# Kernel tuning notes

Hardware: AMD Instinct MI355X
Metric: run time of the kernel (lower is better)

Reference implementation:

```python
import jax, jax.numpy as jnp
import numpy as np

N_NODES = 50000
N_EDGES = 600000
D_IN = 44


def _glorot(key, shape):
    fan_in = shape[0]
    return jax.random.normal(key, shape, jnp.float32) * (1.0 / np.sqrt(fan_in))


def setup_inputs() -> dict:
    key = jax.random.key(0)
    ks = jax.random.split(key, 12)
    x = jax.random.normal(ks[0], (N_NODES, D_IN), jnp.float32)
    edge_index = jax.random.randint(ks[1], (2, N_EDGES), 0, N_NODES, dtype=jnp.int64)
    return {
        "x": x,
        "edge_index": edge_index,
        "W1": _glorot(ks[2], (D_IN, 128)),  "b1": jnp.zeros((128,), jnp.float32),
        "W2": _glorot(ks[3], (128, 64)),    "b2": jnp.zeros((64,), jnp.float32),
        "W3": _glorot(ks[4], (64, 32)),     "b3": jnp.zeros((32,), jnp.float32),
        "Wf1": _glorot(ks[5], (32, 16)),    "bf1": jnp.zeros((16,), jnp.float32),
        "Wf2": _glorot(ks[6], (16, 1)),     "bf2": jnp.zeros((1,), jnp.float32),
    }


def _gcn_conv(x, W, b, src, dst, norm, n):
    # GCNConv: h = x @ W; out_i = sum_{j->i} norm_ij * h_j  (self-loops included in src/dst)
    h = x @ W
    msg = h[src] * norm[:, None]              # [E+N, d_out] gather + scale
    out = jax.ops.segment_sum(msg, dst, num_segments=n)  # scatter-add
    return out + b


def reference(x, edge_index, W1, b1, W2, b2, W3, b3, Wf1, bf1, Wf2, bf2):
    n = x.shape[0]
    loop = jnp.arange(n, dtype=edge_index.dtype)
    src = jnp.concatenate([edge_index[0], loop])
    dst = jnp.concatenate([edge_index[1], loop])
    # symmetric normalization deg^-1/2 A_hat deg^-1/2 (deg includes self-loops)
    deg = jax.ops.segment_sum(jnp.ones_like(dst, dtype=x.dtype), dst, num_segments=n)
    dinv = jax.lax.rsqrt(jnp.maximum(deg, 1.0))
    norm = dinv[src] * dinv[dst]

    h = jax.nn.relu(_gcn_conv(x, W1, b1, src, dst, norm, n))
    h = jax.nn.relu(_gcn_conv(h, W2, b2, src, dst, norm, n))
    h = jax.nn.relu(_gcn_conv(h, W3, b3, src, dst, norm, n))
    h = jax.nn.relu(h @ Wf1 + bf1)
    return jax.nn.sigmoid(h @ Wf2 + bf2)
```

## Files before the change

kernel.cpp:

```cpp
#include <hip/hip_runtime.h>
#include <hip/hip_bf16.h>
#include <hip/hip_fp16.h>
#include <math.h>

#define N_NODES 50000
#define N_EDGES 600000
#define D_IN    44


__device__ __forceinline__ unsigned pack_bf2(float a, float b) {
    unsigned ua = __float_as_uint(a);
    ua = (ua + 0x7fffu + ((ua >> 16) & 1u)) >> 16;
    unsigned ub = __float_as_uint(b);
    ub = (ub + 0x7fffu + ((ub >> 16) & 1u)) & 0xffff0000u;
    return ua | ub;
}


__global__ void k_zero(int* p, int n) {
    int i = blockIdx.x * blockDim.x + threadIdx.x;
    if (i < n) p[i] = 0;
}

__global__ void k_count(const int* __restrict__ dst, int* degc, int e) {
    int i = blockIdx.x * blockDim.x + threadIdx.x;
    if (i < e) atomicAdd(&degc[dst[i]], 1);
}

__global__ void k_blocksum(const int* __restrict__ degc, int* __restrict__ bsum, int n) {
    int i = blockIdx.x * 256 + threadIdx.x;
    int v = (i < n) ? degc[i] : 0;
    #pragma unroll
    for (int off = 32; off > 0; off >>= 1) v += __shfl_down(v, off, 64);
    __shared__ int ws[4];
    if ((threadIdx.x & 63) == 0) ws[threadIdx.x >> 6] = v;
    __syncthreads();
    if (threadIdx.x == 0) bsum[blockIdx.x] = ws[0] + ws[1] + ws[2] + ws[3];
}

__global__ void k_scanbsum(int* bsum, int nb) {
    __shared__ int s[256];
    int t = threadIdx.x;
    int v = (t < nb) ? bsum[t] : 0;
    s[t] = v;
    __syncthreads();
    #pragma unroll
    for (int off = 1; off < 256; off <<= 1) {
        int u = (t >= off) ? s[t - off] : 0;
        __syncthreads();
        s[t] += u;
        __syncthreads();
    }
    if (t < nb) bsum[t] = (t == 0) ? 0 : s[t - 1];
}

__global__ void k_rowptr(const int* __restrict__ degc, const int* __restrict__ bsum,
                         int* __restrict__ row_ptr, int* __restrict__ cursor,
                         float* __restrict__ dinv, int n) {
    __shared__ int s[256];
    int i = blockIdx.x * 256 + threadIdx.x;
    int t = threadIdx.x;
    int d = (i < n) ? degc[i] : 0;
    s[t] = d;
    __syncthreads();
    #pragma unroll
    for (int off = 1; off < 256; off <<= 1) {
        int u = (t >= off) ? s[t - off] : 0;
        __syncthreads();
        s[t] += u;
        __syncthreads();
    }
    int ex = s[t] - d + bsum[blockIdx.x];
    if (i < n) {
        row_ptr[i] = ex;
        cursor[i]  = ex;
        dinv[i]    = rsqrtf(1.0f + (float)d);
        if (i == n - 1) row_ptr[n] = ex + d;
    }
}

__global__ void k_fill(const int* __restrict__ src, const int* __restrict__ dst,
                       const float* __restrict__ dinv, int* cursor,
                       unsigned* __restrict__ csr_ew, int e) {
    int i = blockIdx.x * blockDim.x + threadIdx.x;
    if (i < e) {
        int s = src[i], d = dst[i];
        int p = atomicAdd(&cursor[d], 1);
        __half h = __float2half(dinv[s] * dinv[d]);
        csr_ew[p] = (unsigned)s | ((unsigned)__half_as_ushort(h) << 16);
    }
}

__global__ void k_packx(const float* __restrict__ x, unsigned* __restrict__ xh, int npairs) {
    int i = blockIdx.x * blockDim.x + threadIdx.x;
    if (i < npairs) {
        float2 v = ((const float2*)x)[i];
        xh[i] = pack_bf2(v.x, v.y);
    }
}


#define AGG_BODY(T2, W4, g, j, acc)                                             \
    {                                                                           \
        int lo = row_ptr[g], hi = row_ptr[(g) + 1];                             \
        for (int k = lo; k < hi; k += 8) {                                      \
            unsigned e0 = csr_ew[min(k + 0, hi - 1)];                           \
            unsigned e1 = csr_ew[min(k + 1, hi - 1)];                           \
            unsigned e2 = csr_ew[min(k + 2, hi - 1)];                           \
            unsigned e3 = csr_ew[min(k + 3, hi - 1)];                           \
            unsigned e4 = csr_ew[min(k + 4, hi - 1)];                           \
            unsigned e5 = csr_ew[min(k + 5, hi - 1)];                           \
            unsigned e6 = csr_ew[min(k + 6, hi - 1)];                           \
            unsigned e7 = csr_ew[min(k + 7, hi - 1)];                           \
            float w0 = __half2float(__ushort_as_half((unsigned short)(e0 >> 16)));                     \
            float w1 = (k + 1 < hi) ? __half2float(__ushort_as_half((unsigned short)(e1 >> 16))) : 0.0f;\
            float w2 = (k + 2 < hi) ? __half2float(__ushort_as_half((unsigned short)(e2 >> 16))) : 0.0f;\
            float w3 = (k + 3 < hi) ? __half2float(__ushort_as_half((unsigned short)(e3 >> 16))) : 0.0f;\
            float w4 = (k + 4 < hi) ? __half2float(__ushort_as_half((unsigned short)(e4 >> 16))) : 0.0f;\
            float w5 = (k + 5 < hi) ? __half2float(__ushort_as_half((unsigned short)(e5 >> 16))) : 0.0f;\
            float w6 = (k + 6 < hi) ? __half2float(__ushort_as_half((unsigned short)(e6 >> 16))) : 0.0f;\
            float w7 = (k + 7 < hi) ? __half2float(__ushort_as_half((unsigned short)(e7 >> 16))) : 0.0f;\
            uint2 t0 = T2[(size_t)(e0 & 0xffffu) * (W4) + (j)];                 \
            uint2 t1 = T2[(size_t)(e1 & 0xffffu) * (W4) + (j)];                 \
            uint2 t2 = T2[(size_t)(e2 & 0xffffu) * (W4) + (j)];                 \
            uint2 t3 = T2[(size_t)(e3 & 0xffffu) * (W4) + (j)];                 \
            uint2 t4 = T2[(size_t)(e4 & 0xffffu) * (W4) + (j)];                 \
            uint2 t5 = T2[(size_t)(e5 & 0xffffu) * (W4) + (j)];                 \
            uint2 t6 = T2[(size_t)(e6 & 0xffffu) * (W4) + (j)];                 \
            uint2 t7 = T2[(size_t)(e7 & 0xffffu) * (W4) + (j)];                 \
            AGG_ACC(t0, w0) AGG_ACC(t1, w1) AGG_ACC(t2, w2) AGG_ACC(t3, w3)     \
            AGG_ACC(t4, w4) AGG_ACC(t5, w5) AGG_ACC(t6, w6) AGG_ACC(t7, w7)     \
        }                                                                       \
    }

#define AGG_ACC(tv, wv)                                   \
        acc.x += wv * __uint_as_float(tv.x << 16);        \
        acc.y += wv * __uint_as_float(tv.x & 0xffff0000u);\
        acc.z += wv * __uint_as_float(tv.y << 16);        \
        acc.w += wv * __uint_as_float(tv.y & 0xffff0000u);


__global__ void k_agg1(const unsigned* __restrict__ T, const float* __restrict__ dinv,
                       const int* __restrict__ row_ptr, const unsigned* __restrict__ csr_ew,
                       unsigned short* __restrict__ O, int n) {
    int idx = blockIdx.x * 256 + threadIdx.x;
    if (idx >= n * 11) return;
    int g = idx / 11;
    int j = idx - g * 11;

    const uint2* T2 = (const uint2*)T;
    float di = dinv[g];
    float sw = di * di;
    uint2 sv = T2[(size_t)g * 11 + j];
    float4 acc;
    acc.x = sw * __uint_as_float(sv.x << 16);
    acc.y = sw * __uint_as_float(sv.x & 0xffff0000u);
    acc.z = sw * __uint_as_float(sv.y << 16);
    acc.w = sw * __uint_as_float(sv.y & 0xffff0000u);
    AGG_BODY(T2, 11, g, j, acc)
    uint2 o;
    o.x = pack_bf2(acc.x, acc.y);
    o.y = pack_bf2(acc.z, acc.w);
    ((uint2*)O)[(size_t)g * 11 + j] = o;
}


template<int DI, int DO, int CT, bool BIAS_RELU, bool IN_BF16, bool OUT_BF16>
__global__ void k_gemm(const void* __restrict__ Xv, const float* __restrict__ W,
                       const float* __restrict__ b, void* __restrict__ H, int n) {
    const int ct0 = blockIdx.y * CT;
    int node = blockIdx.x * blockDim.x + threadIdx.x;
    if (node >= n) return;

    float acc[CT];
    #pragma unroll
    for (int c = 0; c < CT; ++c) acc[c] = BIAS_RELU ? b[ct0 + c] : 0.0f;

    const float* Wb = W + ct0;
    #pragma unroll
    for (int k0 = 0; k0 < DI / 4; ++k0) {
        float x0, x1, x2, x3;
        if (IN_BF16) {
            uint2 xv = ((const uint2*)((const unsigned short*)Xv + (size_t)node * DI))[k0];
            x0 = __uint_as_float(xv.x << 16);
            x1 = __uint_as_float(xv.x & 0xffff0000u);
            x2 = __uint_as_float(xv.y << 16);
            x3 = __uint_as_float(xv.y & 0xffff0000u);
        } else {
            float4 xv = ((const float4*)((const float*)Xv + (size_t)node * DI))[k0];
            x0 = xv.x; x1 = xv.y; x2 = xv.z; x3 = xv.w;
        }
        #pragma unroll
        for (int c = 0; c < CT; ++c) acc[c] += x0 * Wb[(k0 * 4 + 0) * DO + c];
        #pragma unroll
        for (int c = 0; c < CT; ++c) acc[c] += x1 * Wb[(k0 * 4 + 1) * DO + c];
        #pragma unroll
        for (int c = 0; c < CT; ++c) acc[c] += x2 * Wb[(k0 * 4 + 2) * DO + c];
        #pragma unroll
        for (int c = 0; c < CT; ++c) acc[c] += x3 * Wb[(k0 * 4 + 3) * DO + c];
    }

    #pragma unroll
    for (int c4 = 0; c4 < CT / 4; ++c4) {
        float4 v;
        v.x = acc[c4 * 4 + 0]; v.y = acc[c4 * 4 + 1];
        v.z = acc[c4 * 4 + 2]; v.w = acc[c4 * 4 + 3];
        if (BIAS_RELU) {
            v.x = fmaxf(v.x, 0.0f); v.y = fmaxf(v.y, 0.0f);
            v.z = fmaxf(v.z, 0.0f); v.w = fmaxf(v.w, 0.0f);
        }
        if (OUT_BF16) {
            uint2 p;
            p.x = pack_bf2(v.x, v.y);
            p.y = pack_bf2(v.z, v.w);
            ((uint2*)((unsigned short*)H + (size_t)node * DO + ct0))[c4] = p;
        } else {
            ((float4*)((float*)H + (size_t)node * DO + ct0))[c4] = v;
        }
    }
}


__global__ void __launch_bounds__(64) k_fused23(
        const unsigned* __restrict__ T, const float* __restrict__ dinv,
        const int* __restrict__ row_ptr, const unsigned* __restrict__ csr_ew,
        const float* __restrict__ b2, const float* __restrict__ W3,
        unsigned short* __restrict__ outH, int n) {
    __shared__ float Xs[4 * 68];
    const int m = threadIdx.x / 16;
    const int j = threadIdx.x % 16;
    const int g = blockIdx.x * 4 + m;
    const int gm = min(g, n - 1);

    const uint2* T2 = (const uint2*)T;
    {
        float di = dinv[gm];
        float sw = di * di;
        uint2 sv = T2[(size_t)gm * 16 + j];
        float4 acc;
        acc.x = sw * __uint_as_float(sv.x << 16);
        acc.y = sw * __uint_as_float(sv.x & 0xffff0000u);
        acc.z = sw * __uint_as_float(sv.y << 16);
        acc.w = sw * __uint_as_float(sv.y & 0xffff0000u);
        AGG_BODY(T2, 16, gm, j, acc)
        float4 bv = ((const float4*)b2)[j];
        acc.x = fmaxf(acc.x + bv.x, 0.0f);
        acc.y = fmaxf(acc.y + bv.y, 0.0f);
        acc.z = fmaxf(acc.z + bv.z, 0.0f);
        acc.w = fmaxf(acc.w + bv.w, 0.0f);
        *(float4*)&Xs[m * 68 + 4 * j] = acc;
    }
    __syncthreads();

    {
        const int c = j * 2;
        float ax = 0.0f, ay = 0.0f;
        #pragma unroll 4
        for (int k4 = 0; k4 < 16; ++k4) {
            float4 hv = *(const float4*)&Xs[m * 68 + 4 * k4];
#define F3_STEP(hs, kk) { \
            float2 wv = *(const float2*)&W3[(kk) * 32 + c]; \
            ax += (hs) * wv.x; ay += (hs) * wv.y; }
            F3_STEP(hv.x, 4 * k4 + 0)
            F3_STEP(hv.y, 4 * k4 + 1)
            F3_STEP(hv.z, 4 * k4 + 2)
            F3_STEP(hv.w, 4 * k4 + 3)
#undef F3_STEP
        }
        if (g < n) *(unsigned*)(outH + (size_t)g * 32 + c) = pack_bf2(ax, ay);
    }
}


__global__ void __launch_bounds__(64) k_fused3m(
        const unsigned* __restrict__ T, const float* __restrict__ dinv,
        const int* __restrict__ row_ptr, const unsigned* __restrict__ csr_ew,
        const float* __restrict__ b3,
        const float* __restrict__ Wf1, const float* __restrict__ bf1,
        const float* __restrict__ Wf2, const float* __restrict__ bf2,
        float* __restrict__ out, int n) {
    __shared__ float Xs[8 * 36];
    const int m = threadIdx.x / 8;
    const int j = threadIdx.x % 8;
    const int g = blockIdx.x * 8 + m;
    const int gm = min(g, n - 1);

    const uint2* T2 = (const uint2*)T;
    {
        float di = dinv[gm];
        float sw = di * di;
        uint2 sv = T2[(size_t)gm * 8 + j];
        float4 acc;
        acc.x = sw * __uint_as_float(sv.x << 16);
        acc.y = sw * __uint_as_float(sv.x & 0xffff0000u);
        acc.z = sw * __uint_as_float(sv.y << 16);
        acc.w = sw * __uint_as_float(sv.y & 0xffff0000u);
        AGG_BODY(T2, 8, gm, j, acc)
        float4 bv = ((const float4*)b3)[j];
        acc.x = fmaxf(acc.x + bv.x, 0.0f);
        acc.y = fmaxf(acc.y + bv.y, 0.0f);
        acc.z = fmaxf(acc.z + bv.z, 0.0f);
        acc.w = fmaxf(acc.w + bv.w, 0.0f);
        *(float4*)&Xs[m * 36 + 4 * j] = acc;
    }
    __syncthreads();

    {
        const int c = j * 2;
        float h0 = bf1[c], h1 = bf1[c + 1];
        #pragma unroll
        for (int k = 0; k < 32; ++k) {
            float xs = Xs[m * 36 + k];
            float2 wv = *(const float2*)&Wf1[k * 16 + c];
            h0 += xs * wv.x;
            h1 += xs * wv.y;
        }
        float2 w2 = *(const float2*)&Wf2[c];
        float partial = fmaxf(h0, 0.0f) * w2.x + fmaxf(h1, 0.0f) * w2.y;
        partial += __shfl_down(partial, 4);
        partial += __shfl_down(partial, 2);
        partial += __shfl_down(partial, 1);
        if (j == 0 && g < n) out[g] = 1.0f / (1.0f + expf(-(partial + bf2[0])));
    }
}


extern "C" void kernel_launch(void* const* d_in, const int* in_sizes, int n_in,
                              void* d_out, int out_size, void* d_ws, size_t ws_size,
                              hipStream_t stream) {
    const float* x   = (const float*)d_in[0];
    const int*   ei  = (const int*)d_in[1];
    const float* W1  = (const float*)d_in[2];
    const float* b1  = (const float*)d_in[3];
    const float* W2  = (const float*)d_in[4];
    const float* b2  = (const float*)d_in[5];
    const float* W3  = (const float*)d_in[6];
    const float* b3  = (const float*)d_in[7];
    const float* Wf1 = (const float*)d_in[8];
    const float* bf1 = (const float*)d_in[9];
    const float* Wf2 = (const float*)d_in[10];
    const float* bf2 = (const float*)d_in[11];
    float* out = (float*)d_out;

    const int N = N_NODES, E = N_EDGES;
    const int* src = ei;
    const int* dst = ei + E;

    const int B   = 256;
    const int NB  = (N + B - 1) / B;
    const int NBX = 200;

    char* w = (char*)d_ws;
    float*    dinv    = (float*)w;     w += (size_t)N * 4;
    int*      degc    = (int*)w;       w += (size_t)N * 4;
    int*      row_ptr = (int*)w;       w += (size_t)(N + 4) * 4;
    int*      cursor  = (int*)w;       w += (size_t)N * 4;
    int*      bsum    = (int*)w;       w += (size_t)256 * 4;
    unsigned* csr_ew  = (unsigned*)w;  w += (size_t)E * 4;
    unsigned* xh      = (unsigned*)w;  w += (size_t)N * 44 * 2;
    unsigned short* aggXh = (unsigned short*)w;  w += (size_t)N * 44 * 2;
    float*    buf1    = (float*)w;     w += (size_t)N * 128 * 4;
    unsigned short* bufAh = (unsigned short*)w;  w += (size_t)N * 64 * 2;
    unsigned short* bufBh = (unsigned short*)w;  w += (size_t)N * 32 * 2;

    k_zero     <<<NB, B, 0, stream>>>(degc, N);
    k_packx    <<<(N * 22 + B - 1) / B, B, 0, stream>>>(x, xh, N * 22);
    k_count    <<<(E + B - 1) / B, B, 0, stream>>>(dst, degc, E);
    k_blocksum <<<NB, B, 0, stream>>>(degc, bsum, N);
    k_scanbsum <<<1, B, 0, stream>>>(bsum, NB);
    k_rowptr   <<<NB, B, 0, stream>>>(degc, bsum, row_ptr, cursor, dinv, N);
    k_fill     <<<(E + B - 1) / B, B, 0, stream>>>(src, dst, dinv, cursor, csr_ew, E);

    k_agg1<<<(N * 11 + B - 1) / B, B, 0, stream>>>(xh, dinv, row_ptr, csr_ew, aggXh, N);
    k_gemm<44, 128, 16, true, true, false><<<dim3(NBX, 8), B, 0, stream>>>(aggXh, W1, b1, buf1, N);
    k_gemm<128, 64, 16, false, false, true><<<dim3(NBX, 4), B, 0, stream>>>(buf1, W2, nullptr, bufAh, N);

    k_fused23<<<(N + 3) / 4, 64, 0, stream>>>((const unsigned*)bufAh, dinv, row_ptr,
                                              csr_ew, b2, W3, bufBh, N);

    k_fused3m<<<(N + 7) / 8, 64, 0, stream>>>((const unsigned*)bufBh, dinv, row_ptr,
                                              csr_ew, b3, Wf1, bf1, Wf2, bf2, out, N);
}
```

Measured before the change: 263.1 us.

## Widen aggregation gathers to 16-byte loads, enlarge fused blocks, merge setup kernels

In the layer-2/3 fused kernels, each thread now gathers a uint4 (8 bf16 values) per neighbour instead of a uint2, which halves the threads per node. Blocks are enlarged to 32 nodes each, and each thread computes 4 output columns in the small GEMM epilogue. Separately, the degree zeroing is folded into the x-packing kernel and the block-sum scan into the row-pointer kernel, removing two launches. The tradeoffs are more registers per thread and a redundant 256-wide scan in every row-pointer block.

```diff
diff --git a/kernel.cpp b/kernel.cpp
--- a/kernel.cpp
+++ b/kernel.cpp
@@ -16,10 +16,18 @@
     return ua | ub;
 }
 
-
-__global__ void k_zero(int* p, int n) {
+#define BL(u) __uint_as_float((u) << 16)
+#define BH(u) __uint_as_float((u) & 0xffff0000u)
+
+
+__global__ void k_packx(const float* __restrict__ x, unsigned* __restrict__ xh,
+                        int npairs, int* __restrict__ degc, int n) {
     int i = blockIdx.x * blockDim.x + threadIdx.x;
-    if (i < n) p[i] = 0;
+    if (i < npairs) {
+        float2 v = ((const float2*)x)[i];
+        xh[i] = pack_bf2(v.x, v.y);
+    }
+    if (i < n) degc[i] = 0;
 }
 
 __global__ void k_count(const int* __restrict__ dst, int* degc, int e) {
@@ -38,11 +46,28 @@
     if (threadIdx.x == 0) bsum[blockIdx.x] = ws[0] + ws[1] + ws[2] + ws[3];
 }
 
-__global__ void k_scanbsum(int* bsum, int nb) {
+__global__ void k_rowptr(const int* __restrict__ degc, const int* __restrict__ bsum,
+                         int* __restrict__ row_ptr, int* __restrict__ cursor,
+                         float* __restrict__ dinv, int n, int nb) {
+    __shared__ int sb[256];
     __shared__ int s[256];
     int t = threadIdx.x;
-    int v = (t < nb) ? bsum[t] : 0;
-    s[t] = v;
+
+    int bv = (t < nb) ? bsum[t] : 0;
+    sb[t] = bv;
+    __syncthreads();
+    #pragma unroll
+    for (int off = 1; off < 256; off <<= 1) {
+        int u = (t >= off) ? sb[t - off] : 0;
+        __syncthreads();
+        sb[t] += u;
+        __syncthreads();
+    }
+    int prefix = (blockIdx.x == 0) ? 0 : sb[blockIdx.x - 1];
+
+    int i = blockIdx.x * 256 + t;
+    int d = (i < n) ? degc[i] : 0;
+    s[t] = d;
     __syncthreads();
     #pragma unroll
     for (int off = 1; off < 256; off <<= 1) {
@@ -51,26 +76,7 @@
         s[t] += u;
         __syncthreads();
     }
-    if (t < nb) bsum[t] = (t == 0) ? 0 : s[t - 1];
-}
-
-__global__ void k_rowptr(const int* __restrict__ degc, const int* __restrict__ bsum,
-                         int* __restrict__ row_ptr, int* __restrict__ cursor,
-                         float* __restrict__ dinv, int n) {
-    __shared__ int s[256];
-    int i = blockIdx.x * 256 + threadIdx.x;
-    int t = threadIdx.x;
-    int d = (i < n) ? degc[i] : 0;
-    s[t] = d;
-    __syncthreads();
-    #pragma unroll
-    for (int off = 1; off < 256; off <<= 1) {
-        int u = (t >= off) ? s[t - off] : 0;
-        __syncthreads();
-        s[t] += u;
-        __syncthreads();
-    }
-    int ex = s[t] - d + bsum[blockIdx.x];
+    int ex = s[t] - d + prefix;
     if (i < n) {
         row_ptr[i] = ex;
         cursor[i]  = ex;
@@ -88,14 +94,6 @@
         int p = atomicAdd(&cursor[d], 1);
         __half h = __float2half(dinv[s] * dinv[d]);
         csr_ew[p] = (unsigned)s | ((unsigned)__half_as_ushort(h) << 16);
-    }
-}
-
-__global__ void k_packx(const float* __restrict__ x, unsigned* __restrict__ xh, int npairs) {
-    int i = blockIdx.x * blockDim.x + threadIdx.x;
-    if (i < npairs) {
-        float2 v = ((const float2*)x)[i];
-        xh[i] = pack_bf2(v.x, v.y);
     }
 }
 
@@ -134,10 +132,50 @@
     }
 
 #define AGG_ACC(tv, wv)                                   \
-        acc.x += wv * __uint_as_float(tv.x << 16);        \
-        acc.y += wv * __uint_as_float(tv.x & 0xffff0000u);\
-        acc.z += wv * __uint_as_float(tv.y << 16);        \
-        acc.w += wv * __uint_as_float(tv.y & 0xffff0000u);
+        acc.x += wv * BL(tv.x);                           \
+        acc.y += wv * BH(tv.x);                           \
+        acc.z += wv * BL(tv.y);                           \
+        acc.w += wv * BH(tv.y);
+
+
+#define AGG_ACC4(tv, wv)                                  \
+        a0.x += wv * BL(tv.x); a0.y += wv * BH(tv.x);     \
+        a0.z += wv * BL(tv.y); a0.w += wv * BH(tv.y);     \
+        a1.x += wv * BL(tv.z); a1.y += wv * BH(tv.z);     \
+        a1.z += wv * BL(tv.w); a1.w += wv * BH(tv.w);
+
+#define AGG_BODY4(T4, W4, g, j)                                                 \
+    {                                                                           \
+        int lo = row_ptr[g], hi = row_ptr[(g) + 1];                             \
+        for (int k = lo; k < hi; k += 8) {                                      \
+            unsigned e0 = csr_ew[min(k + 0, hi - 1)];                           \
+            unsigned e1 = csr_ew[min(k + 1, hi - 1)];                           \
+            unsigned e2 = csr_ew[min(k + 2, hi - 1)];                           \
+            unsigned e3 = csr_ew[min(k + 3, hi - 1)];                           \
+            unsigned e4 = csr_ew[min(k + 4, hi - 1)];                           \
+            unsigned e5 = csr_ew[min(k + 5, hi - 1)];                           \
+            unsigned e6 = csr_ew[min(k + 6, hi - 1)];                           \
+            unsigned e7 = csr_ew[min(k + 7, hi - 1)];                           \
+            float w0 = __half2float(__ushort_as_half((unsigned short)(e0 >> 16)));                     \
+            float w1 = (k + 1 < hi) ? __half2float(__ushort_as_half((unsigned short)(e1 >> 16))) : 0.0f;\
+            float w2 = (k + 2 < hi) ? __half2float(__ushort_as_half((unsigned short)(e2 >> 16))) : 0.0f;\
+            float w3 = (k + 3 < hi) ? __half2float(__ushort_as_half((unsigned short)(e3 >> 16))) : 0.0f;\
+            float w4 = (k + 4 < hi) ? __half2float(__ushort_as_half((unsigned short)(e4 >> 16))) : 0.0f;\
+            float w5 = (k + 5 < hi) ? __half2float(__ushort_as_half((unsigned short)(e5 >> 16))) : 0.0f;\
+            float w6 = (k + 6 < hi) ? __half2float(__ushort_as_half((unsigned short)(e6 >> 16))) : 0.0f;\
+            float w7 = (k + 7 < hi) ? __half2float(__ushort_as_half((unsigned short)(e7 >> 16))) : 0.0f;\
+            uint4 t0 = T4[(size_t)(e0 & 0xffffu) * (W4) + (j)];                 \
+            uint4 t1 = T4[(size_t)(e1 & 0xffffu) * (W4) + (j)];                 \
+            uint4 t2 = T4[(size_t)(e2 & 0xffffu) * (W4) + (j)];                 \
+            uint4 t3 = T4[(size_t)(e3 & 0xffffu) * (W4) + (j)];                 \
+            uint4 t4 = T4[(size_t)(e4 & 0xffffu) * (W4) + (j)];                 \
+            uint4 t5 = T4[(size_t)(e5 & 0xffffu) * (W4) + (j)];                 \
+            uint4 t6 = T4[(size_t)(e6 & 0xffffu) * (W4) + (j)];                 \
+            uint4 t7 = T4[(size_t)(e7 & 0xffffu) * (W4) + (j)];                 \
+            AGG_ACC4(t0, w0) AGG_ACC4(t1, w1) AGG_ACC4(t2, w2) AGG_ACC4(t3, w3) \
+            AGG_ACC4(t4, w4) AGG_ACC4(t5, w5) AGG_ACC4(t6, w6) AGG_ACC4(t7, w7) \
+        }                                                                       \
+    }
 
 
 __global__ void k_agg1(const unsigned* __restrict__ T, const float* __restrict__ dinv,
@@ -153,10 +191,10 @@
     float sw = di * di;
     uint2 sv = T2[(size_t)g * 11 + j];
     float4 acc;
-    acc.x = sw * __uint_as_float(sv.x << 16);
-    acc.y = sw * __uint_as_float(sv.x & 0xffff0000u);
-    acc.z = sw * __uint_as_float(sv.y << 16);
-    acc.w = sw * __uint_as_float(sv.y & 0xffff0000u);
+    acc.x = sw * BL(sv.x);
+    acc.y = sw * BH(sv.x);
+    acc.z = sw * BL(sv.y);
+    acc.w = sw * BH(sv.y);
     AGG_BODY(T2, 11, g, j, acc)
     uint2 o;
     o.x = pack_bf2(acc.x, acc.y);
@@ -182,10 +220,7 @@
         float x0, x1, x2, x3;
         if (IN_BF16) {
             uint2 xv = ((const uint2*)((const unsigned short*)Xv + (size_t)node * DI))[k0];
-            x0 = __uint_as_float(xv.x << 16);
-            x1 = __uint_as_float(xv.x & 0xffff0000u);
-            x2 = __uint_as_float(xv.y << 16);
-            x3 = __uint_as_float(xv.y & 0xffff0000u);
+            x0 = BL(xv.x); x1 = BH(xv.x); x2 = BL(xv.y); x3 = BH(xv.y);
         } else {
             float4 xv = ((const float4*)((const float*)Xv + (size_t)node * DI))[k0];
             x0 = xv.x; x1 = xv.y; x2 = xv.z; x3 = xv.w;
@@ -221,106 +256,118 @@
 }
 
 
-__global__ void __launch_bounds__(64) k_fused23(
+__global__ void __launch_bounds__(256) k_fused23(
         const unsigned* __restrict__ T, const float* __restrict__ dinv,
         const int* __restrict__ row_ptr, const unsigned* __restrict__ csr_ew,
         const float* __restrict__ b2, const float* __restrict__ W3,
         unsigned short* __restrict__ outH, int n) {
-    __shared__ float Xs[4 * 68];
-    const int m = threadIdx.x / 16;
-    const int j = threadIdx.x % 16;
-    const int g = blockIdx.x * 4 + m;
+    __shared__ float Xs[32 * 68];
+    const int t = threadIdx.x;
+    const int m = t >> 3;
+    const int j = t & 7;
+    const int g = blockIdx.x * 32 + m;
     const int gm = min(g, n - 1);
 
-    const uint2* T2 = (const uint2*)T;
+    const uint4* T4 = (const uint4*)T;
     {
         float di = dinv[gm];
         float sw = di * di;
-        uint2 sv = T2[(size_t)gm * 16 + j];
-        float4 acc;
-        acc.x = sw * __uint_as_float(sv.x << 16);
-        acc.y = sw * __uint_as_float(sv.x & 0xffff0000u);
-        acc.z = sw * __uint_as_float(sv.y << 16);
-        acc.w = sw * __uint_as_float(sv.y & 0xffff0000u);
-        AGG_BODY(T2, 16, gm, j, acc)
-        float4 bv = ((const float4*)b2)[j];
-        acc.x = fmaxf(acc.x + bv.x, 0.0f);
-        acc.y = fmaxf(acc.y + bv.y, 0.0f);
-        acc.z = fmaxf(acc.z + bv.z, 0.0f);
-        acc.w = fmaxf(acc.w + bv.w, 0.0f);
-        *(float4*)&Xs[m * 68 + 4 * j] = acc;
+        uint4 sv = T4[(size_t)gm * 8 + j];
+        float4 a0, a1;
+        a0.x = sw * BL(sv.x); a0.y = sw * BH(sv.x);
+        a0.z = sw * BL(sv.y); a0.w = sw * BH(sv.y);
+        a1.x = sw * BL(sv.z); a1.y = sw * BH(sv.z);
+        a1.z = sw * BL(sv.w); a1.w = sw * BH(sv.w);
+        AGG_BODY4(T4, 8, gm, j)
+        float4 bv0 = ((const float4*)b2)[2 * j];
+        float4 bv1 = ((const float4*)b2)[2 * j + 1];
+        a0.x = fmaxf(a0.x + bv0.x, 0.0f); a0.y = fmaxf(a0.y + bv0.y, 0.0f);
+        a0.z = fmaxf(a0.z + bv0.z, 0.0f); a0.w = fmaxf(a0.w + bv0.w, 0.0f);
+        a1.x = fmaxf(a1.x + bv1.x, 0.0f); a1.y = fmaxf(a1.y + bv1.y, 0.0f);
+        a1.z = fmaxf(a1.z + bv1.z, 0.0f); a1.w = fmaxf(a1.w + bv1.w, 0.0f);
+        *(float4*)&Xs[m * 68 + 8 * j]     = a0;
+        *(float4*)&Xs[m * 68 + 8 * j + 4] = a1;
     }
     __syncthreads();
 
     {
-        const int c = j * 2;
-        float ax = 0.0f, ay = 0.0f;
+        const int c = j * 4;
+        float4 o = {0.0f, 0.0f, 0.0f, 0.0f};
         #pragma unroll 4
         for (int k4 = 0; k4 < 16; ++k4) {
-            float4 hv = *(const float4*)&Xs[m * 68 + 4 * k4];
-#define F3_STEP(hs, kk) { \
-            float2 wv = *(const float2*)&W3[(kk) * 32 + c]; \
-            ax += (hs) * wv.x; ay += (hs) * wv.y; }
-            F3_STEP(hv.x, 4 * k4 + 0)
-            F3_STEP(hv.y, 4 * k4 + 1)
-            F3_STEP(hv.z, 4 * k4 + 2)
-            F3_STEP(hv.w, 4 * k4 + 3)
-#undef F3_STEP
-        }
-        if (g < n) *(unsigned*)(outH + (size_t)g * 32 + c) = pack_bf2(ax, ay);
-    }
-}
-
-
-__global__ void __launch_bounds__(64) k_fused3m(
+            float4 xs = *(const float4*)&Xs[m * 68 + 4 * k4];
+#define G3(hs, kk) { float4 wv = *(const float4*)&W3[(kk) * 32 + c];            \
+            o.x += (hs) * wv.x; o.y += (hs) * wv.y;                             \
+            o.z += (hs) * wv.z; o.w += (hs) * wv.w; }
+            G3(xs.x, 4 * k4 + 0) G3(xs.y, 4 * k4 + 1)
+            G3(xs.z, 4 * k4 + 2) G3(xs.w, 4 * k4 + 3)
+#undef G3
+        }
+        if (g < n) {
+            uint2 ov;
+            ov.x = pack_bf2(o.x, o.y);
+            ov.y = pack_bf2(o.z, o.w);
+            *(uint2*)(outH + (size_t)g * 32 + c) = ov;
+        }
+    }
+}
+
+
+__global__ void __launch_bounds__(128) k_fused3m(
         const unsigned* __restrict__ T, const float* __restrict__ dinv,
         const int* __restrict__ row_ptr, const unsigned* __restrict__ csr_ew,
         const float* __restrict__ b3,
         const float* __restrict__ Wf1, const float* __restrict__ bf1,
         const float* __restrict__ Wf2, const float* __restrict__ bf2,
         float* __restrict__ out, int n) {
-    __shared__ float Xs[8 * 36];
-    const int m = threadIdx.x / 8;
-    const int j = threadIdx.x % 8;
-    const int g = blockIdx.x * 8 + m;
+    __shared__ float Xs[32 * 36];
+    const int t = threadIdx.x;
+    const int m = t >> 2;
+    const int j = t & 3;
+    const int g = blockIdx.x * 32 + m;
     const int gm = min(g, n - 1);
 
-    const uint2* T2 = (const uint2*)T;
+    const uint4* T4 = (const uint4*)T;
     {
         float di = dinv[gm];
         float sw = di * di;
-        uint2 sv = T2[(size_t)gm * 8 + j];
-        float4 acc;
-        acc.x = sw * __uint_as_float(sv.x << 16);
-        acc.y = sw * __uint_as_float(sv.x & 0xffff0000u);
-        acc.z = sw * __uint_as_float(sv.y << 16);
-        acc.w = sw * __uint_as_float(sv.y & 0xffff0000u);
-        AGG_BODY(T2, 8, gm, j, acc)
-        float4 bv = ((const float4*)b3)[j];
-        acc.x = fmaxf(acc.x + bv.x, 0.0f);
-        acc.y = fmaxf(acc.y + bv.y, 0.0f);
-        acc.z = fmaxf(acc.z + bv.z, 0.0f);
-        acc.w = fmaxf(acc.w + bv.w, 0.0f);
-        *(float4*)&Xs[m * 36 + 4 * j] = acc;
+        uint4 sv = T4[(size_t)gm * 4 + j];
+        float4 a0, a1;
+        a0.x = sw * BL(sv.x); a0.y = sw * BH(sv.x);
+        a0.z = sw * BL(sv.y); a0.w = sw * BH(sv.y);
+        a1.x = sw * BL(sv.z); a1.y = sw * BH(sv.z);
+        a1.z = sw * BL(sv.w); a1.w = sw * BH(sv.w);
+        AGG_BODY4(T4, 4, gm, j)
+        float4 bv0 = ((const float4*)b3)[2 * j];
+        float4 bv1 = ((const float4*)b3)[2 * j + 1];
+        a0.x = fmaxf(a0.x + bv0.x, 0.0f); a0.y = fmaxf(a0.y + bv0.y, 0.0f);
+        a0.z = fmaxf(a0.z + bv0.z, 0.0f); a0.w = fmaxf(a0.w + bv0.w, 0.0f);
+        a1.x = fmaxf(a1.x + bv1.x, 0.0f); a1.y = fmaxf(a1.y + bv1.y, 0.0f);
+        a1.z = fmaxf(a1.z + bv1.z, 0.0f); a1.w = fmaxf(a1.w + bv1.w, 0.0f);
+        *(float4*)&Xs[m * 36 + 8 * j]     = a0;
+        *(float4*)&Xs[m * 36 + 8 * j + 4] = a1;
     }
     __syncthreads();
 
     {
-        const int c = j * 2;
-        float h0 = bf1[c], h1 = bf1[c + 1];
+        const int c = j * 4;
+        float4 h = *(const float4*)&bf1[c];
         #pragma unroll
-        for (int k = 0; k < 32; ++k) {
-            float xs = Xs[m * 36 + k];
-            float2 wv = *(const float2*)&Wf1[k * 16 + c];
-            h0 += xs * wv.x;
-            h1 += xs * wv.y;
-        }
-        float2 w2 = *(const float2*)&Wf2[c];
-        float partial = fmaxf(h0, 0.0f) * w2.x + fmaxf(h1, 0.0f) * w2.y;
-        partial += __shfl_down(partial, 4);
-        partial += __shfl_down(partial, 2);
-        partial += __shfl_down(partial, 1);
-        if (j == 0 && g < n) out[g] = 1.0f / (1.0f + expf(-(partial + bf2[0])));
+        for (int k4 = 0; k4 < 8; ++k4) {
+            float4 xs = *(const float4*)&Xs[m * 36 + 4 * k4];
+#define FM(hs, kk) { float4 wv = *(const float4*)&Wf1[(kk) * 16 + c];           \
+            h.x += (hs) * wv.x; h.y += (hs) * wv.y;                             \
+            h.z += (hs) * wv.z; h.w += (hs) * wv.w; }
+            FM(xs.x, 4 * k4 + 0) FM(xs.y, 4 * k4 + 1)
+            FM(xs.z, 4 * k4 + 2) FM(xs.w, 4 * k4 + 3)
+#undef FM
+        }
+        float4 w2 = *(const float4*)&Wf2[c];
+        float p = fmaxf(h.x, 0.0f) * w2.x + fmaxf(h.y, 0.0f) * w2.y
+                + fmaxf(h.z, 0.0f) * w2.z + fmaxf(h.w, 0.0f) * w2.w;
+        p += __shfl_down(p, 2);
+        p += __shfl_down(p, 1);
+        if (j == 0 && g < n) out[g] = 1.0f / (1.0f + expf(-(p + bf2[0])));
     }
 }
 
@@ -363,21 +410,19 @@
     unsigned short* bufAh = (unsigned short*)w;  w += (size_t)N * 64 * 2;
     unsigned short* bufBh = (unsigned short*)w;  w += (size_t)N * 32 * 2;
 
-    k_zero     <<<NB, B, 0, stream>>>(degc, N);
-    k_packx    <<<(N * 22 + B - 1) / B, B, 0, stream>>>(x, xh, N * 22);
+    k_packx    <<<(N * 22 + B - 1) / B, B, 0, stream>>>(x, xh, N * 22, degc, N);
     k_count    <<<(E + B - 1) / B, B, 0, stream>>>(dst, degc, E);
     k_blocksum <<<NB, B, 0, stream>>>(degc, bsum, N);
-    k_scanbsum <<<1, B, 0, stream>>>(bsum, NB);
-    k_rowptr   <<<NB, B, 0, stream>>>(degc, bsum, row_ptr, cursor, dinv, N);
+    k_rowptr   <<<NB, B, 0, stream>>>(degc, bsum, row_ptr, cursor, dinv, N, NB);
     k_fill     <<<(E + B - 1) / B, B, 0, stream>>>(src, dst, dinv, cursor, csr_ew, E);
 
     k_agg1<<<(N * 11 + B - 1) / B, B, 0, stream>>>(xh, dinv, row_ptr, csr_ew, aggXh, N);
     k_gemm<44, 128, 16, true, true, false><<<dim3(NBX, 8), B, 0, stream>>>(aggXh, W1, b1, buf1, N);
     k_gemm<128, 64, 16, false, false, true><<<dim3(NBX, 4), B, 0, stream>>>(buf1, W2, nullptr, bufAh, N);
 
-    k_fused23<<<(N + 3) / 4, 64, 0, stream>>>((const unsigned*)bufAh, dinv, row_ptr,
-                                              csr_ew, b2, W3, bufBh, N);
-
-    k_fused3m<<<(N + 7) / 8, 64, 0, stream>>>((const unsigned*)bufBh, dinv, row_ptr,
-                                              csr_ew, b3, Wf1, bf1, Wf2, bf2, out, N);
-}
+    k_fused23<<<(N + 31) / 32, 256, 0, stream>>>((const unsigned*)bufAh, dinv, row_ptr,
+                                                 csr_ew, b2, W3, bufBh, N);
+
+    k_fused3m<<<(N + 31) / 32, 128, 0, stream>>>((const unsigned*)bufBh, dinv, row_ptr,
+                                                 csr_ew, b3, Wf1, bf1, Wf2, bf2, out, N);
+}
```

After: 246.7 us. 6.3% less time.
